# Kernel tuning notes

Measured on AMD Instinct MI355X. Metric: run time of the kernel, lower is better.

## Reference

```python
import jax, jax.numpy as jnp
import numpy as np

B, H, M_DIM, K, N = 4, 8, 2048, 2048, 64
NNZ = B * H * M_DIM * 64


def setup_inputs() -> dict:
    key = jax.random.key(0)
    k_val, k_b, k_bh, k_m, k_k = jax.random.split(key, 5)
    values = jax.random.normal(k_val, (NNZ,), dtype=jnp.float32)
    b = jax.random.normal(k_b, (B, H, K, N), dtype=jnp.float32)
    idx_bh = jax.random.randint(k_bh, (NNZ,), 0, B * H, dtype=jnp.int32)
    idx_m = jax.random.randint(k_m, (NNZ,), 0, M_DIM, dtype=jnp.int32)
    idx_k = jax.random.randint(k_k, (NNZ,), 0, K, dtype=jnp.int32)
    return {"values": values, "b": b, "idx_bh": idx_bh, "idx_m": idx_m,
            "idx_k": idx_k, "M": M_DIM}


def reference(values, b, idx_bh, idx_m, idx_k, M):
    # Batched sparse-dense matmul: out[b,h,m,:] = sum_k A[b,h,m,k] * b[b,h,k,:]
    # A is in COO form over flattened batch-head dim: (idx_bh, idx_m, idx_k, values).
    Bd, Hd, Kd, Nd = b.shape
    b_flat = b.reshape(Bd * Hd, Kd, Nd)             # [BH, K, N]
    # gather the dense rows each nonzero touches, scale by the sparse value
    gathered = values[:, None] * b_flat[idx_bh, idx_k]  # [nnz, N]
    # scatter-add into output rows (flat segment id = bh*M + m)
    seg = idx_bh * M + idx_m
    out = jax.ops.segment_sum(gathered, seg, num_segments=Bd * Hd * M)  # [BH*M, N]
    return out.reshape(Bd, Hd, M, Nd)
```

## Files before the change

kernel.cpp:

```cpp
#include <hip/hip_runtime.h>

constexpr int N_COLS = 64;
constexpr int K_DIM  = 2048;
constexpr int M_DIM  = 2048;
constexpr int SEGS   = 32 * 2048;
constexpr int NBUCK  = 512;
constexpr int SEG_PER_BUCK = SEGS / NBUCK;
constexpr int PART_T = 1024;
constexpr int PART_E = 8;
constexpr int TILE   = PART_T * PART_E;
constexpr int CAP    = 8960;
constexpr int OSTR   = 520;


__global__ void spmm_coo_atomic(const float* __restrict__ values,
                                const float* __restrict__ b,
                                const int*   __restrict__ idx_bh,
                                const int*   __restrict__ idx_m,
                                const int*   __restrict__ idx_k,
                                float*       __restrict__ out,
                                int nnz) {
    long long gid = (long long)blockIdx.x * blockDim.x + threadIdx.x;
    int nz   = (int)(gid >> 6);
    int lane = (int)(gid & 63);
    if (nz >= nnz) return;
    float bval = b[((size_t)idx_bh[nz] * K_DIM + idx_k[nz]) * N_COLS + lane];
    atomicAdd(&out[((size_t)idx_bh[nz] * M_DIM + idx_m[nz]) * N_COLS + lane],
              values[nz] * bval);
}

__global__ __launch_bounds__(PART_T)
void partition512(const float* __restrict__ values,
                  const int*   __restrict__ idx_bh,
                  const int*   __restrict__ idx_m,
                  const int*   __restrict__ idx_k,
                  const float* __restrict__ b,
                  unsigned int* __restrict__ bbf,
                  int*  __restrict__ offt,
                  int*  __restrict__ tiles,
                  int nnz, int nblk) {
    __shared__ int ebuf[TILE];
    __shared__ int lcount[NBUCK];
    __shared__ int sc[NBUCK];
    __shared__ int lstart[NBUCK];
    __shared__ int total_s;

    int t   = threadIdx.x;
    int bid = blockIdx.x;

    for (int sl = bid; sl < 512; sl += nblk) {
        size_t base = (size_t)sl * 8192 + (size_t)t * 8;
        const float4* s = (const float4*)(b + base);
        float4 x = s[0], y = s[1];
        auto cv = [](float a, float c) {
            unsigned ua = __float_as_uint(a), uc = __float_as_uint(c);
            ua = (ua + 0x7FFFu + ((ua >> 16) & 1u)) >> 16;
            uc = (uc + 0x7FFFu + ((uc >> 16) & 1u)) >> 16;
            return ua | (uc << 16);
        };
        uint4 r = make_uint4(cv(x.x, x.y), cv(x.z, x.w), cv(y.x, y.y), cv(y.z, y.w));
        *(uint4*)(bbf + base / 2) = r;
    }

    if (t < NBUCK) lcount[t] = 0;
    __syncthreads();

    int e0 = bid * TILE + t * PART_E;
    int   pk[PART_E];
    short bkt[PART_E];
    short rnk[PART_E];

    auto enc = [](int vb, int k, int seg) {
        return (int)(((unsigned)(vb + 0x20000) & 0xFFFC0000u) | ((unsigned)k << 7)
                     | ((unsigned)seg & 127u));
    };

    if (e0 + PART_E <= nnz) {
        const int4* vv4 = (const int4*)(values + e0);
        const int4* bh4 = (const int4*)(idx_bh + e0);
        const int4* mm4 = (const int4*)(idx_m + e0);
        const int4* kk4 = (const int4*)(idx_k + e0);
        #pragma unroll
        for (int q = 0; q < PART_E / 4; ++q) {
            int4 vq = vv4[q];
            int4 bq = bh4[q], mq = mm4[q], kq = kk4[q];
            int s0 = bq.x * M_DIM + mq.x;
            int s1 = bq.y * M_DIM + mq.y;
            int s2 = bq.z * M_DIM + mq.z;
            int s3 = bq.w * M_DIM + mq.w;
            pk[4*q+0]=enc(vq.x,kq.x,s0); bkt[4*q+0]=(short)(s0>>7);
            rnk[4*q+0]=(short)atomicAdd(&lcount[s0>>7],1);
            pk[4*q+1]=enc(vq.y,kq.y,s1); bkt[4*q+1]=(short)(s1>>7);
            rnk[4*q+1]=(short)atomicAdd(&lcount[s1>>7],1);
            pk[4*q+2]=enc(vq.z,kq.z,s2); bkt[4*q+2]=(short)(s2>>7);
            rnk[4*q+2]=(short)atomicAdd(&lcount[s2>>7],1);
            pk[4*q+3]=enc(vq.w,kq.w,s3); bkt[4*q+3]=(short)(s3>>7);
            rnk[4*q+3]=(short)atomicAdd(&lcount[s3>>7],1);
        }
    } else {
        #pragma unroll
        for (int i = 0; i < PART_E; ++i) {
            int e = e0 + i;
            if (e < nnz) {
                int seg = idx_bh[e] * M_DIM + idx_m[e];
                int bu  = seg >> 7;
                pk[i]  = enc(__float_as_int(values[e]), idx_k[e], seg);
                bkt[i] = (short)bu;
                rnk[i] = (short)atomicAdd(&lcount[bu], 1);
            } else bkt[i] = -1;
        }
    }
    __syncthreads();

    int c = (t < NBUCK) ? lcount[t] : 0;

    if (t < NBUCK) sc[t] = c;
    __syncthreads();
    for (int d = 1; d < NBUCK; d <<= 1) {
        int x = 0;
        if (t < NBUCK && t >= d) x = sc[t - d];
        __syncthreads();
        if (t < NBUCK && t >= d) sc[t] += x;
        __syncthreads();
    }
    if (t < NBUCK) {
        int ls = sc[t] - c;
        lstart[t] = ls;
        if (t == NBUCK - 1) total_s = sc[t];
    }
    __syncthreads();

    if (t < NBUCK) offt[(size_t)bid * OSTR + t] = lstart[t];
    if (t == NBUCK) offt[(size_t)bid * OSTR + NBUCK] = total_s;

    #pragma unroll
    for (int i = 0; i < PART_E; ++i) {
        if (bkt[i] >= 0)
            ebuf[lstart[bkt[i]] + rnk[i]] = pk[i];
    }
    __syncthreads();

    int4* tp = (int4*)(tiles + (size_t)bid * TILE);
    const int4* eb4 = (const int4*)ebuf;
    tp[t]        = eb4[t];
    tp[t + 1024] = eb4[t + 1024];
}

__global__ __launch_bounds__(1024)
void sort_accum(const int* __restrict__ tiles,
                const int* __restrict__ offt,
                const unsigned short* __restrict__ bbf,
                float* __restrict__ out, int nblk) {
    __shared__ int stage[CAP];
    __shared__ int ps[CAP + 8];
    __shared__ int h[SEG_PER_BUCK];
    __shared__ int cur[SEG_PER_BUCK];
    __shared__ int sc[NBUCK];
    __shared__ int pf[NBUCK + 1];
    __shared__ int ro[NBUCK];

    int t = threadIdx.x;
    int i   = blockIdx.x;
    int bkt = (i & 7) * 64 + (i >> 3);

    if (t < SEG_PER_BUCK) h[t] = 0;

    int cA = 0, cB = 0;
    if (t < NBUCK) {
        if (t < nblk) {
            cA = offt[(size_t)t * OSTR + bkt];
            cB = offt[(size_t)t * OSTR + bkt + 1];
        }
        ro[t] = cA;
        sc[t] = cB - cA;
    }
    __syncthreads();
    for (int d = 1; d < NBUCK; d <<= 1) {
        int x = 0;
        if (t < NBUCK && t >= d) x = sc[t - d];
        __syncthreads();
        if (t < NBUCK && t >= d) sc[t] += x;
        __syncthreads();
    }
    if (t < NBUCK) {
        pf[t + 1] = sc[t];
        if (t == 0) pf[0] = 0;
    }
    __syncthreads();

    int lane = t & 63;
    int w    = t >> 6;
    for (int r = 0; r < 32; ++r) {
        int bsrc = w * 32 + r;
        int s0  = pf[bsrc];
        int len = pf[bsrc + 1] - s0;
        const int* src = tiles + (size_t)bsrc * TILE + ro[bsrc];
        for (int e = lane; e < len; e += 64) {
            int val = src[e];
            int dst = s0 + e;
            if (dst < CAP) {
                stage[dst] = val;
                atomicAdd(&h[val & 127], 1);
            }
        }
    }
    __syncthreads();

    int Lt = pf[NBUCK];
    if (Lt > CAP) Lt = CAP;

    for (int d = 1; d < SEG_PER_BUCK; d <<= 1) {
        int x = 0;
        if (t < SEG_PER_BUCK && t >= d) x = h[t - d];
        __syncthreads();
        if (t < SEG_PER_BUCK && t >= d) h[t] += x;
        __syncthreads();
    }
    if (t < SEG_PER_BUCK) cur[t] = (t == 0) ? 0 : h[t - 1];
    __syncthreads();

    for (int idx = t; idx < Lt; idx += 1024) {
        int e = stage[idx];
        int pos = atomicAdd(&cur[e & 127], 1);
        ps[pos] = e;
    }
    __syncthreads();
    if (t < 8) ps[Lt + t] = 0;
    __syncthreads();

    int bh = bkt >> 4;
    const char* bb = (const char*)bbf + ((size_t)bh << 18);
    size_t obase = ((size_t)bkt << 13);
    int lb = lane * 2;

    for (int s = w * 8; s < w * 8 + 8; ++s) {
        int js = (s == 0) ? 0 : h[s - 1];
        int je = h[s];
        float a0 = 0.f, a1 = 0.f, a2 = 0.f, a3 = 0.f;
        int j = js;
        for (; j + 8 <= je; j += 8) {
            int s0 = __builtin_amdgcn_readfirstlane(ps[j+0]);
            int s1 = __builtin_amdgcn_readfirstlane(ps[j+1]);
            int s2 = __builtin_amdgcn_readfirstlane(ps[j+2]);
            int s3 = __builtin_amdgcn_readfirstlane(ps[j+3]);
            int s4 = __builtin_amdgcn_readfirstlane(ps[j+4]);
            int s5 = __builtin_amdgcn_readfirstlane(ps[j+5]);
            int s6 = __builtin_amdgcn_readfirstlane(ps[j+6]);
            int s7 = __builtin_amdgcn_readfirstlane(ps[j+7]);
            unsigned short u0 = *(const unsigned short*)(bb + (s0 & 0x3FF80) + lb);
            unsigned short u1 = *(const unsigned short*)(bb + (s1 & 0x3FF80) + lb);
            unsigned short u2 = *(const unsigned short*)(bb + (s2 & 0x3FF80) + lb);
            unsigned short u3 = *(const unsigned short*)(bb + (s3 & 0x3FF80) + lb);
            unsigned short u4 = *(const unsigned short*)(bb + (s4 & 0x3FF80) + lb);
            unsigned short u5 = *(const unsigned short*)(bb + (s5 & 0x3FF80) + lb);
            unsigned short u6 = *(const unsigned short*)(bb + (s6 & 0x3FF80) + lb);
            unsigned short u7 = *(const unsigned short*)(bb + (s7 & 0x3FF80) + lb);
            a0 += __int_as_float(s0 & (int)0xFFFC0000) * __int_as_float((int)u0 << 16);
            a1 += __int_as_float(s1 & (int)0xFFFC0000) * __int_as_float((int)u1 << 16);
            a2 += __int_as_float(s2 & (int)0xFFFC0000) * __int_as_float((int)u2 << 16);
            a3 += __int_as_float(s3 & (int)0xFFFC0000) * __int_as_float((int)u3 << 16);
            a0 += __int_as_float(s4 & (int)0xFFFC0000) * __int_as_float((int)u4 << 16);
            a1 += __int_as_float(s5 & (int)0xFFFC0000) * __int_as_float((int)u5 << 16);
            a2 += __int_as_float(s6 & (int)0xFFFC0000) * __int_as_float((int)u6 << 16);
            a3 += __int_as_float(s7 & (int)0xFFFC0000) * __int_as_float((int)u7 << 16);
        }
        if (j < je) {
            int s0 = __builtin_amdgcn_readfirstlane(ps[j+0]);
            int s1 = __builtin_amdgcn_readfirstlane(ps[j+1]);
            int s2 = __builtin_amdgcn_readfirstlane(ps[j+2]);
            int s3 = __builtin_amdgcn_readfirstlane(ps[j+3]);
            int s4 = __builtin_amdgcn_readfirstlane(ps[j+4]);
            int s5 = __builtin_amdgcn_readfirstlane(ps[j+5]);
            int s6 = __builtin_amdgcn_readfirstlane(ps[j+6]);
            int s7 = __builtin_amdgcn_readfirstlane(ps[j+7]);
            unsigned short u0 = *(const unsigned short*)(bb + (s0 & 0x3FF80) + lb);
            unsigned short u1 = *(const unsigned short*)(bb + (s1 & 0x3FF80) + lb);
            unsigned short u2 = *(const unsigned short*)(bb + (s2 & 0x3FF80) + lb);
            unsigned short u3 = *(const unsigned short*)(bb + (s3 & 0x3FF80) + lb);
            unsigned short u4 = *(const unsigned short*)(bb + (s4 & 0x3FF80) + lb);
            unsigned short u5 = *(const unsigned short*)(bb + (s5 & 0x3FF80) + lb);
            unsigned short u6 = *(const unsigned short*)(bb + (s6 & 0x3FF80) + lb);
            unsigned short u7 = *(const unsigned short*)(bb + (s7 & 0x3FF80) + lb);
            float v0 = (j+0 < je) ? __int_as_float(s0 & (int)0xFFFC0000) : 0.f;
            float v1 = (j+1 < je) ? __int_as_float(s1 & (int)0xFFFC0000) : 0.f;
            float v2 = (j+2 < je) ? __int_as_float(s2 & (int)0xFFFC0000) : 0.f;
            float v3 = (j+3 < je) ? __int_as_float(s3 & (int)0xFFFC0000) : 0.f;
            float v4 = (j+4 < je) ? __int_as_float(s4 & (int)0xFFFC0000) : 0.f;
            float v5 = (j+5 < je) ? __int_as_float(s5 & (int)0xFFFC0000) : 0.f;
            float v6 = (j+6 < je) ? __int_as_float(s6 & (int)0xFFFC0000) : 0.f;
            float v7 = (j+7 < je) ? __int_as_float(s7 & (int)0xFFFC0000) : 0.f;
            a0 += v0 * __int_as_float((int)u0 << 16);
            a1 += v1 * __int_as_float((int)u1 << 16);
            a2 += v2 * __int_as_float((int)u2 << 16);
            a3 += v3 * __int_as_float((int)u3 << 16);
            a0 += v4 * __int_as_float((int)u4 << 16);
            a1 += v5 * __int_as_float((int)u5 << 16);
            a2 += v6 * __int_as_float((int)u6 << 16);
            a3 += v7 * __int_as_float((int)u7 << 16);
        }
        out[obase + ((size_t)s << 6) + lane] = (a0 + a1) + (a2 + a3);
    }
}

extern "C" void kernel_launch(void* const* d_in, const int* in_sizes, int n_in,
                              void* d_out, int out_size, void* d_ws, size_t ws_size,
                              hipStream_t stream) {
    const float* values = (const float*)d_in[0];
    const float* b      = (const float*)d_in[1];
    const int*   idx_bh = (const int*)d_in[2];
    const int*   idx_m  = (const int*)d_in[3];
    const int*   idx_k  = (const int*)d_in[4];
    float*       out    = (float*)d_out;
    const int    nnz    = in_sizes[0];

    const int nblk = (nnz + TILE - 1) / TILE;

    const size_t offt_sz   = (size_t)nblk * OSTR * sizeof(int);
    const size_t bbf_off   = (offt_sz + 255) & ~(size_t)255;
    const size_t tiles_off = bbf_off + 8388608;
    const size_t need      = tiles_off + (size_t)nblk * TILE * sizeof(int);

    int* offt = (int*)d_ws;
    unsigned int* bbf = (unsigned int*)((char*)d_ws + bbf_off);
    int* tiles = (int*)((char*)d_ws + tiles_off);

    if (ws_size >= need && nblk <= NBUCK) {
        partition512<<<nblk, PART_T, 0, stream>>>(values, idx_bh, idx_m, idx_k,
                                                  b, bbf, offt, tiles, nnz, nblk);
        sort_accum<<<NBUCK, 1024, 0, stream>>>(tiles, offt,
                                               (const unsigned short*)bbf, out, nblk);
    } else {
        hipMemsetAsync(d_out, 0, (size_t)out_size * sizeof(float), stream);
        long long total = (long long)nnz * N_COLS;
        spmm_coo_atomic<<<(unsigned)((total + 255) / 256), 256, 0, stream>>>(
            values, b, idx_bh, idx_m, idx_k, out, nnz);
    }
}
```

Before: 184.4 us.

## Drop shared staging buffer and pad segments to eight for vector LDS reads

The accumulation kernel no longer copies each bucket's entries into a shared staging array. It now reads the tile entries from global memory twice: once to build the per-segment histogram and once to scatter entries into sorted order. Segment lengths are rounded up to multiples of eight, and the padding is zero-filled, so the inner loop reads eight entries with two int4 shared loads and needs no masked tail. This saves shared memory and removes the tail branch, but costs a second pass over global tile data, a shared-memory clear, and extra padded iterations.

Measured after the change: 174.6 us (median of 2 runs). 5.3% less time.

```diff
diff --git a/kernel.cpp b/kernel.cpp
--- a/kernel.cpp
+++ b/kernel.cpp
@@ -10,6 +10,7 @@
 constexpr int PART_E = 8;
 constexpr int TILE   = PART_T * PART_E;
 constexpr int CAP    = 8960;
+constexpr int PS_CAP = CAP + SEG_PER_BUCK * 7;
 constexpr int OSTR   = 520;
 
 
@@ -151,19 +152,24 @@
                 const int* __restrict__ offt,
                 const unsigned short* __restrict__ bbf,
                 float* __restrict__ out, int nblk) {
-    __shared__ int stage[CAP];
-    __shared__ int ps[CAP + 8];
+    __shared__ int4 ps4[PS_CAP / 4];
     __shared__ int h[SEG_PER_BUCK];
     __shared__ int cur[SEG_PER_BUCK];
     __shared__ int sc[NBUCK];
     __shared__ int pf[NBUCK + 1];
     __shared__ int ro[NBUCK];
+    int* ps = (int*)ps4;
 
     int t = threadIdx.x;
     int i   = blockIdx.x;
     int bkt = (i & 7) * 64 + (i >> 3);
 
     if (t < SEG_PER_BUCK) h[t] = 0;
+    #pragma unroll
+    for (int q = 0; q < 3; ++q) {
+        int idx = t + q * 1024;
+        if (idx < PS_CAP / 4) ps4[idx] = make_int4(0, 0, 0, 0);
+    }
 
     int cA = 0, cB = 0;
     if (t < NBUCK) {
@@ -190,25 +196,20 @@
 
     int lane = t & 63;
     int w    = t >> 6;
-    for (int r = 0; r < 32; ++r) {
-        int bsrc = w * 32 + r;
-        int s0  = pf[bsrc];
-        int len = pf[bsrc + 1] - s0;
+    int lg   = lane >> 4;
+    int li   = lane & 15;
+
+    for (int r = 0; r < 32; r += 4) {
+        int bsrc = w * 32 + r + lg;
+        int len = pf[bsrc + 1] - pf[bsrc];
         const int* src = tiles + (size_t)bsrc * TILE + ro[bsrc];
-        for (int e = lane; e < len; e += 64) {
-            int val = src[e];
-            int dst = s0 + e;
-            if (dst < CAP) {
-                stage[dst] = val;
-                atomicAdd(&h[val & 127], 1);
-            }
-        }
-    }
-    __syncthreads();
-
-    int Lt = pf[NBUCK];
-    if (Lt > CAP) Lt = CAP;
-
+        for (int e = li; e < len; e += 16)
+            atomicAdd(&h[src[e] & 127], 1);
+    }
+    __syncthreads();
+
+    if (t < SEG_PER_BUCK) h[t] = (h[t] + 7) & ~7;
+    __syncthreads();
     for (int d = 1; d < SEG_PER_BUCK; d <<= 1) {
         int x = 0;
         if (t < SEG_PER_BUCK && t >= d) x = h[t - d];
@@ -216,16 +217,21 @@
         if (t < SEG_PER_BUCK && t >= d) h[t] += x;
         __syncthreads();
     }
+    if (t < SEG_PER_BUCK) { if (h[t] > PS_CAP) h[t] = PS_CAP; }
+    __syncthreads();
     if (t < SEG_PER_BUCK) cur[t] = (t == 0) ? 0 : h[t - 1];
     __syncthreads();
 
-    for (int idx = t; idx < Lt; idx += 1024) {
-        int e = stage[idx];
-        int pos = atomicAdd(&cur[e & 127], 1);
-        ps[pos] = e;
-    }
-    __syncthreads();
-    if (t < 8) ps[Lt + t] = 0;
+    for (int r = 0; r < 32; r += 4) {
+        int bsrc = w * 32 + r + lg;
+        int len = pf[bsrc + 1] - pf[bsrc];
+        const int* src = tiles + (size_t)bsrc * TILE + ro[bsrc];
+        for (int e = li; e < len; e += 16) {
+            int val = src[e];
+            int pos = atomicAdd(&cur[val & 127], 1);
+            if (pos < PS_CAP) ps[pos] = val;
+        }
+    }
     __syncthreads();
 
     int bh = bkt >> 4;
@@ -237,16 +243,17 @@
         int js = (s == 0) ? 0 : h[s - 1];
         int je = h[s];
         float a0 = 0.f, a1 = 0.f, a2 = 0.f, a3 = 0.f;
-        int j = js;
-        for (; j + 8 <= je; j += 8) {
-            int s0 = __builtin_amdgcn_readfirstlane(ps[j+0]);
-            int s1 = __builtin_amdgcn_readfirstlane(ps[j+1]);
-            int s2 = __builtin_amdgcn_readfirstlane(ps[j+2]);
-            int s3 = __builtin_amdgcn_readfirstlane(ps[j+3]);
-            int s4 = __builtin_amdgcn_readfirstlane(ps[j+4]);
-            int s5 = __builtin_amdgcn_readfirstlane(ps[j+5]);
-            int s6 = __builtin_amdgcn_readfirstlane(ps[j+6]);
-            int s7 = __builtin_amdgcn_readfirstlane(ps[j+7]);
+        for (int j = js; j < je; j += 8) {
+            int4 g0 = *(const int4*)&ps[j];
+            int4 g1 = *(const int4*)&ps[j + 4];
+            int s0 = __builtin_amdgcn_readfirstlane(g0.x);
+            int s1 = __builtin_amdgcn_readfirstlane(g0.y);
+            int s2 = __builtin_amdgcn_readfirstlane(g0.z);
+            int s3 = __builtin_amdgcn_readfirstlane(g0.w);
+            int s4 = __builtin_amdgcn_readfirstlane(g1.x);
+            int s5 = __builtin_amdgcn_readfirstlane(g1.y);
+            int s6 = __builtin_amdgcn_readfirstlane(g1.z);
+            int s7 = __builtin_amdgcn_readfirstlane(g1.w);
             unsigned short u0 = *(const unsigned short*)(bb + (s0 & 0x3FF80) + lb);
             unsigned short u1 = *(const unsigned short*)(bb + (s1 & 0x3FF80) + lb);
             unsigned short u2 = *(const unsigned short*)(bb + (s2 & 0x3FF80) + lb);
@@ -264,40 +271,6 @@
             a2 += __int_as_float(s6 & (int)0xFFFC0000) * __int_as_float((int)u6 << 16);
             a3 += __int_as_float(s7 & (int)0xFFFC0000) * __int_as_float((int)u7 << 16);
         }
-        if (j < je) {
-            int s0 = __builtin_amdgcn_readfirstlane(ps[j+0]);
-            int s1 = __builtin_amdgcn_readfirstlane(ps[j+1]);
-            int s2 = __builtin_amdgcn_readfirstlane(ps[j+2]);
-            int s3 = __builtin_amdgcn_readfirstlane(ps[j+3]);
-            int s4 = __builtin_amdgcn_readfirstlane(ps[j+4]);
-            int s5 = __builtin_amdgcn_readfirstlane(ps[j+5]);
-            int s6 = __builtin_amdgcn_readfirstlane(ps[j+6]);
-            int s7 = __builtin_amdgcn_readfirstlane(ps[j+7]);
-            unsigned short u0 = *(const unsigned short*)(bb + (s0 & 0x3FF80) + lb);
-            unsigned short u1 = *(const unsigned short*)(bb + (s1 & 0x3FF80) + lb);
-            unsigned short u2 = *(const unsigned short*)(bb + (s2 & 0x3FF80) + lb);
-            unsigned short u3 = *(const unsigned short*)(bb + (s3 & 0x3FF80) + lb);
-            unsigned short u4 = *(const unsigned short*)(bb + (s4 & 0x3FF80) + lb);
-            unsigned short u5 = *(const unsigned short*)(bb + (s5 & 0x3FF80) + lb);
-            unsigned short u6 = *(const unsigned short*)(bb + (s6 & 0x3FF80) + lb);
-            unsigned short u7 = *(const unsigned short*)(bb + (s7 & 0x3FF80) + lb);
-            float v0 = (j+0 < je) ? __int_as_float(s0 & (int)0xFFFC0000) : 0.f;
-            float v1 = (j+1 < je) ? __int_as_float(s1 & (int)0xFFFC0000) : 0.f;
-            float v2 = (j+2 < je) ? __int_as_float(s2 & (int)0xFFFC0000) : 0.f;
-            float v3 = (j+3 < je) ? __int_as_float(s3 & (int)0xFFFC0000) : 0.f;
-            float v4 = (j+4 < je) ? __int_as_float(s4 & (int)0xFFFC0000) : 0.f;
-            float v5 = (j+5 < je) ? __int_as_float(s5 & (int)0xFFFC0000) : 0.f;
-            float v6 = (j+6 < je) ? __int_as_float(s6 & (int)0xFFFC0000) : 0.f;
-            float v7 = (j+7 < je) ? __int_as_float(s7 & (int)0xFFFC0000) : 0.f;
-            a0 += v0 * __int_as_float((int)u0 << 16);
-            a1 += v1 * __int_as_float((int)u1 << 16);
-            a2 += v2 * __int_as_float((int)u2 << 16);
-            a3 += v3 * __int_as_float((int)u3 << 16);
-            a0 += v4 * __int_as_float((int)u4 << 16);
-            a1 += v5 * __int_as_float((int)u5 << 16);
-            a2 += v6 * __int_as_float((int)u6 << 16);
-            a3 += v7 * __int_as_float((int)u7 << 16);
-        }
         out[obase + ((size_t)s << 6) + lane] = (a0 + a1) + (a2 + a3);
     }
 }
```
